# Kernel tuning notes

Hardware: AMD Instinct MI355X
Metric: run time of the kernel (lower is better)

Reference implementation:

```python
import jax, jax.numpy as jnp
import numpy as np

MARGIN = 0.2
NEG_INF = -1e30
POS_INF = 1e30


def setup_inputs() -> dict:
    key = jax.random.key(0)
    k1, k2 = jax.random.split(key)
    B, D = 8192, 128
    im = jax.random.normal(k1, (B, D), dtype=jnp.float32)
    ids = jax.random.randint(k2, (B,), 0, 512, dtype=jnp.int64)
    return {"im": im, "ids": ids}


def reference(im, ids):
    # scores[i, j] = <im_i, im_j>, with the diagonal zeroed (as in the original,
    # which sets scores[j][j] = 0 before mining). Note the positive set includes
    # the anchor itself, so min over positives includes the zeroed diagonal.
    B = im.shape[0]
    scores = im @ im.T                      # [B, B]
    scores = scores * (1.0 - jnp.eye(B, dtype=scores.dtype))
    pos_mask = ids[:, None] == ids[None, :]  # same id (includes self)
    neg_mask = ~pos_mask
    max_neg = jnp.max(jnp.where(neg_mask, scores, NEG_INF), axis=1)  # hardest negative per anchor
    min_pos = jnp.min(jnp.where(pos_mask, scores, POS_INF), axis=1)  # hardest positive per anchor
    cost = jnp.sum(jnp.maximum(MARGIN + max_neg - min_pos, 0.0))
    return cost
```

## Files before the change

kernel.cpp:

```cpp
#include <hip/hip_runtime.h>
#include <hip/hip_bf16.h>

#define MARGIN  0.2f
#define NEG_INF -1e30f
#define POS_INF 1e30f

#define B_SZ 8192
#define D_SZ 128
#define CS   16
#define BLK_COLS 512
#define PHASE_COLS 64
#define NPH (BLK_COLS / PHASE_COLS)

typedef __bf16 bf16x8 __attribute__((ext_vector_type(8)));
typedef __bf16 bf16x4 __attribute__((ext_vector_type(4)));
typedef float  f32x4  __attribute__((ext_vector_type(4)));

__global__ __launch_bounds__(256) void k_convert(const float* __restrict__ in,
                                                 __bf16* __restrict__ out) {
    int i = (blockIdx.x * 256 + threadIdx.x) * 4;
    float4 v = *reinterpret_cast<const float4*>(in + i);
    bf16x4 o;
    o[0] = (__bf16)v.x; o[1] = (__bf16)v.y; o[2] = (__bf16)v.z; o[3] = (__bf16)v.w;
    *reinterpret_cast<bf16x4*>(out + i) = o;
}

__global__ __launch_bounds__(256, 3) void k_mine(const __bf16* __restrict__ imb,
                                                 const int* __restrict__ ids,
                                                 float* __restrict__ wsmax,
                                                 float* __restrict__ wsmin) {
    __shared__ __bf16 bpanel[2][PHASE_COLS * D_SZ];
    __shared__ int    ids_s[BLK_COLS];

    const int bid = blockIdx.x;
    const int wg  = (bid & 7) * 64 + (bid >> 3);
    const int rb  = wg & 31;
    const int cs  = wg >> 5;

    const int tid  = threadIdx.x;
    const int w    = tid >> 6;
    const int lane = tid & 63;
    const int quad = lane >> 4;
    const int lr   = lane & 15;

    const int rowbase = rb * 256 + w * 64;
    const int col0    = cs * BLK_COLS;

    bf16x8 afrag[4][4];
    #pragma unroll
    for (int s = 0; s < 4; ++s) {
        const __bf16* p = imb + (size_t)(rowbase + s * 16 + lr) * D_SZ + quad * 8;
        #pragma unroll
        for (int kf = 0; kf < 4; ++kf)
            afrag[s][kf] = *reinterpret_cast<const bf16x8*>(p + kf * 32);
    }

    int rid[4][4];
    #pragma unroll
    for (int s = 0; s < 4; ++s)
        #pragma unroll
        for (int r = 0; r < 4; ++r)
            rid[s][r] = ids[rowbase + s * 16 + quad * 4 + r];

    int2 myids = *reinterpret_cast<const int2*>(ids + col0 + tid * 2);
    *reinterpret_cast<int2*>(&ids_s[tid * 2]) = myids;

    {
        const __bf16* src = imb + (size_t)(col0 + w * 16 + lr) * D_SZ + quad * 8;
        #pragma unroll
        for (int kf = 0; kf < 4; ++kf)
            __builtin_amdgcn_global_load_lds(
                (const __attribute__((address_space(1))) unsigned int*)(src + kf * 32),
                (__attribute__((address_space(3))) unsigned int*)(&bpanel[0][(w * 4 + kf) * 512]),
                16, 0, 0);
    }
    asm volatile("s_waitcnt vmcnt(0) lgkmcnt(0)" ::: "memory");
    __builtin_amdgcn_s_barrier();

    float mxn[4][4], mnp[4][4];
    #pragma unroll
    for (int s = 0; s < 4; ++s)
        #pragma unroll
        for (int r = 0; r < 4; ++r) { mxn[s][r] = NEG_INF; mnp[s][r] = POS_INF; }

    #pragma unroll 1
    for (int p = 0; p < NPH; ++p) {
        if (p + 1 < NPH) {
            const int nbuf = (p + 1) & 1;
            const __bf16* src = imb + (size_t)(col0 + (p + 1) * PHASE_COLS + w * 16 + lr) * D_SZ + quad * 8;
            #pragma unroll
            for (int kf = 0; kf < 4; ++kf)
                __builtin_amdgcn_global_load_lds(
                    (const __attribute__((address_space(1))) unsigned int*)(src + kf * 32),
                    (__attribute__((address_space(3))) unsigned int*)(&bpanel[nbuf][(w * 4 + kf) * 512]),
                    16, 0, 0);
        }
        const int buf = p & 1;
        #pragma unroll 1
        for (int tt = 0; tt < 4; ++tt) {
            const int cid = ids_s[p * PHASE_COLS + tt * 16 + lr];
            bf16x8 bfr[4];
            const __bf16* bp = &bpanel[buf][tt * 4 * 512] + lane * 8;
            #pragma unroll
            for (int kf = 0; kf < 4; ++kf)
                bfr[kf] = *reinterpret_cast<const bf16x8*>(bp + kf * 512);
            #pragma unroll
            for (int s = 0; s < 4; ++s) {
                f32x4 acc = {0.f, 0.f, 0.f, 0.f};
                #pragma unroll
                for (int kf = 0; kf < 4; ++kf)
                    acc = __builtin_amdgcn_mfma_f32_16x16x32_bf16(afrag[s][kf], bfr[kf], acc, 0, 0, 0);
                #pragma unroll
                for (int r = 0; r < 4; ++r) {
                    float sv   = acc[r];
                    bool  same = (rid[s][r] == cid);
                    mxn[s][r] = fmaxf(mxn[s][r], same ? NEG_INF : sv);
                    mnp[s][r] = fminf(mnp[s][r], same ? sv : POS_INF);
                }
            }
        }
        asm volatile("s_waitcnt vmcnt(0) lgkmcnt(0)" ::: "memory");
        __builtin_amdgcn_s_barrier();
    }

    #pragma unroll
    for (int s = 0; s < 4; ++s)
        #pragma unroll
        for (int r = 0; r < 4; ++r) {
            float mx = mxn[s][r];
            float mn = mnp[s][r];
            #pragma unroll
            for (int m = 1; m < 16; m <<= 1) {
                mx = fmaxf(mx, __shfl_xor(mx, m, 64));
                mn = fminf(mn, __shfl_xor(mn, m, 64));
            }
            if (lr == 0) {
                int row = rowbase + s * 16 + quad * 4 + r;
                wsmax[(size_t)row * CS + cs] = mx;
                wsmin[(size_t)row * CS + cs] = mn;
            }
        }
}

__global__ __launch_bounds__(256) void k_final(const float* __restrict__ wsmax,
                                               const float* __restrict__ wsmin,
                                               float* __restrict__ out) {
    int r = blockIdx.x * 256 + threadIdx.x;
    float mx = NEG_INF;
    float mn = 0.0f;
    #pragma unroll
    for (int c = 0; c < CS; c += 4) {
        f32x4 vx = *reinterpret_cast<const f32x4*>(wsmax + (size_t)r * CS + c);
        f32x4 vn = *reinterpret_cast<const f32x4*>(wsmin + (size_t)r * CS + c);
        mx = fmaxf(mx, fmaxf(fmaxf(vx[0], vx[1]), fmaxf(vx[2], vx[3])));
        mn = fminf(mn, fminf(fminf(vn[0], vn[1]), fminf(vn[2], vn[3])));
    }
    float cost = fmaxf(MARGIN + mx - mn, 0.0f);
    #pragma unroll
    for (int m = 1; m < 64; m <<= 1)
        cost += __shfl_xor(cost, m, 64);
    __shared__ float part[4];
    if ((threadIdx.x & 63) == 0) part[threadIdx.x >> 6] = cost;
    __syncthreads();
    if (threadIdx.x == 0)
        atomicAdd(out, part[0] + part[1] + part[2] + part[3]);
}

extern "C" void kernel_launch(void* const* d_in, const int* in_sizes, int n_in,
                              void* d_out, int out_size, void* d_ws, size_t ws_size,
                              hipStream_t stream) {
    const float* im  = (const float*)d_in[0];
    const int*   ids = (const int*)d_in[1];
    float*       out = (float*)d_out;

    __bf16* imb   = (__bf16*)d_ws;
    float*  wsmax = (float*)((char*)d_ws + (size_t)B_SZ * D_SZ * 2);
    float*  wsmin = wsmax + (size_t)B_SZ * CS;

    hipMemsetAsync(d_out, 0, sizeof(float), stream);

    k_convert<<<(B_SZ * D_SZ) / (256 * 4), 256, 0, stream>>>(im, imb);
    k_mine<<<32 * CS, 256, 0, stream>>>(imb, ids, wsmax, wsmin);
    k_final<<<B_SZ / 256, 256, 0, stream>>>(wsmax, wsmin, out);
}
```

Before: 100.4 us.

## Switch mining kernel to 32x32x16 MFMA with 128-row blocks

Replaces the 16x16x32 MFMA tiling with 32x32x16 bf16 MFMA. Each wave now owns 32 rows with 16 accumulator values, and blocks cover 128 rows, so the grid doubles to 1024 workgroups. The B-panel LDS layout and ids mapping are reworked to match the 32x32 fragment layout, and the tt loop is unrolled. The aim is fewer MFMA issues per output plus more blocks for occupancy, at the cost of reloading the B panel for twice as many row blocks. The convert kernel also widens to 8 elements per thread and the final kernel uses 128-thread blocks.

Result: no change. 98.60 us (-1.8%).

```diff
diff --git a/kernel.cpp b/kernel.cpp
--- a/kernel.cpp
+++ b/kernel.cpp
@@ -13,16 +13,18 @@
 #define NPH (BLK_COLS / PHASE_COLS)
 
 typedef __bf16 bf16x8 __attribute__((ext_vector_type(8)));
-typedef __bf16 bf16x4 __attribute__((ext_vector_type(4)));
 typedef float  f32x4  __attribute__((ext_vector_type(4)));
+typedef float  f32x16 __attribute__((ext_vector_type(16)));
 
 __global__ __launch_bounds__(256) void k_convert(const float* __restrict__ in,
                                                  __bf16* __restrict__ out) {
-    int i = (blockIdx.x * 256 + threadIdx.x) * 4;
-    float4 v = *reinterpret_cast<const float4*>(in + i);
-    bf16x4 o;
-    o[0] = (__bf16)v.x; o[1] = (__bf16)v.y; o[2] = (__bf16)v.z; o[3] = (__bf16)v.w;
-    *reinterpret_cast<bf16x4*>(out + i) = o;
+    int i = (blockIdx.x * 256 + threadIdx.x) * 8;
+    float4 v0 = *reinterpret_cast<const float4*>(in + i);
+    float4 v1 = *reinterpret_cast<const float4*>(in + i + 4);
+    bf16x8 o;
+    o[0] = (__bf16)v0.x; o[1] = (__bf16)v0.y; o[2] = (__bf16)v0.z; o[3] = (__bf16)v0.w;
+    o[4] = (__bf16)v1.x; o[5] = (__bf16)v1.y; o[6] = (__bf16)v1.z; o[7] = (__bf16)v1.w;
+    *reinterpret_cast<bf16x8*>(out + i) = o;
 }
 
 __global__ __launch_bounds__(256, 3) void k_mine(const __bf16* __restrict__ imb,
@@ -33,90 +35,85 @@
     __shared__ int    ids_s[BLK_COLS];
 
     const int bid = blockIdx.x;
-    const int wg  = (bid & 7) * 64 + (bid >> 3);
-    const int rb  = wg & 31;
-    const int cs  = wg >> 5;
+    const int wg  = (bid & 7) * 128 + (bid >> 3);
+    const int rb  = wg & 63;
+    const int cs  = wg >> 6;
 
     const int tid  = threadIdx.x;
     const int w    = tid >> 6;
     const int lane = tid & 63;
-    const int quad = lane >> 4;
-    const int lr   = lane & 15;
+    const int half = lane >> 5;
+    const int l5   = lane & 31;
 
-    const int rowbase = rb * 256 + w * 64;
+    const int rowbase = rb * 128 + w * 32;
     const int col0    = cs * BLK_COLS;
 
-    bf16x8 afrag[4][4];
-    #pragma unroll
-    for (int s = 0; s < 4; ++s) {
-        const __bf16* p = imb + (size_t)(rowbase + s * 16 + lr) * D_SZ + quad * 8;
+    const int s_tile = w >> 1;
+    const int s_kf0  = (w & 1) * 4;
+
+    {
+        const __bf16* src = imb + (size_t)(col0 + s_tile * 32 + l5) * D_SZ + s_kf0 * 16 + half * 8;
         #pragma unroll
-        for (int kf = 0; kf < 4; ++kf)
-            afrag[s][kf] = *reinterpret_cast<const bf16x8*>(p + kf * 32);
+        for (int j = 0; j < 4; ++j)
+            __builtin_amdgcn_global_load_lds(
+                (const __attribute__((address_space(1))) unsigned int*)(src + j * 16),
+                (__attribute__((address_space(3))) unsigned int*)(&bpanel[0][(s_tile * 8 + s_kf0 + j) * 512]),
+                16, 0, 0);
     }
 
-    int rid[4][4];
+    bf16x8 afrag[8];
+    {
+        const __bf16* p = imb + (size_t)(rowbase + l5) * D_SZ + half * 8;
+        #pragma unroll
+        for (int kf = 0; kf < 8; ++kf)
+            afrag[kf] = *reinterpret_cast<const bf16x8*>(p + kf * 16);
+    }
+
+    int rid[16];
     #pragma unroll
-    for (int s = 0; s < 4; ++s)
-        #pragma unroll
-        for (int r = 0; r < 4; ++r)
-            rid[s][r] = ids[rowbase + s * 16 + quad * 4 + r];
+    for (int r = 0; r < 16; ++r)
+        rid[r] = ids[rowbase + (r & 3) + 8 * (r >> 2) + 4 * half];
 
-    int2 myids = *reinterpret_cast<const int2*>(ids + col0 + tid * 2);
-    *reinterpret_cast<int2*>(&ids_s[tid * 2]) = myids;
+    *reinterpret_cast<int2*>(&ids_s[tid * 2]) =
+        *reinterpret_cast<const int2*>(ids + col0 + tid * 2);
 
-    {
-        const __bf16* src = imb + (size_t)(col0 + w * 16 + lr) * D_SZ + quad * 8;
-        #pragma unroll
-        for (int kf = 0; kf < 4; ++kf)
-            __builtin_amdgcn_global_load_lds(
-                (const __attribute__((address_space(1))) unsigned int*)(src + kf * 32),
-                (__attribute__((address_space(3))) unsigned int*)(&bpanel[0][(w * 4 + kf) * 512]),
-                16, 0, 0);
-    }
     asm volatile("s_waitcnt vmcnt(0) lgkmcnt(0)" ::: "memory");
     __builtin_amdgcn_s_barrier();
 
-    float mxn[4][4], mnp[4][4];
+    float mxn[16], mnp[16];
     #pragma unroll
-    for (int s = 0; s < 4; ++s)
-        #pragma unroll
-        for (int r = 0; r < 4; ++r) { mxn[s][r] = NEG_INF; mnp[s][r] = POS_INF; }
+    for (int r = 0; r < 16; ++r) { mxn[r] = NEG_INF; mnp[r] = POS_INF; }
 
     #pragma unroll 1
     for (int p = 0; p < NPH; ++p) {
         if (p + 1 < NPH) {
             const int nbuf = (p + 1) & 1;
-            const __bf16* src = imb + (size_t)(col0 + (p + 1) * PHASE_COLS + w * 16 + lr) * D_SZ + quad * 8;
+            const __bf16* src = imb + (size_t)(col0 + (p + 1) * PHASE_COLS + s_tile * 32 + l5) * D_SZ
+                                + s_kf0 * 16 + half * 8;
             #pragma unroll
-            for (int kf = 0; kf < 4; ++kf)
+            for (int j = 0; j < 4; ++j)
                 __builtin_amdgcn_global_load_lds(
-                    (const __attribute__((address_space(1))) unsigned int*)(src + kf * 32),
-                    (__attribute__((address_space(3))) unsigned int*)(&bpanel[nbuf][(w * 4 + kf) * 512]),
+                    (const __attribute__((address_space(1))) unsigned int*)(src + j * 16),
+                    (__attribute__((address_space(3))) unsigned int*)(&bpanel[nbuf][(s_tile * 8 + s_kf0 + j) * 512]),
                     16, 0, 0);
         }
         const int buf = p & 1;
-        #pragma unroll 1
-        for (int tt = 0; tt < 4; ++tt) {
-            const int cid = ids_s[p * PHASE_COLS + tt * 16 + lr];
-            bf16x8 bfr[4];
-            const __bf16* bp = &bpanel[buf][tt * 4 * 512] + lane * 8;
+        #pragma unroll
+        for (int t = 0; t < 2; ++t) {
+            const __bf16* bbase = &bpanel[buf][t * 4096] + (size_t)lane * 8;
+            f32x16 acc = {};
             #pragma unroll
-            for (int kf = 0; kf < 4; ++kf)
-                bfr[kf] = *reinterpret_cast<const bf16x8*>(bp + kf * 512);
+            for (int kf = 0; kf < 8; ++kf) {
+                bf16x8 bfr = *reinterpret_cast<const bf16x8*>(bbase + kf * 512);
+                acc = __builtin_amdgcn_mfma_f32_32x32x16_bf16(afrag[kf], bfr, acc, 0, 0, 0);
+            }
+            const int cid = ids_s[p * PHASE_COLS + t * 32 + l5];
             #pragma unroll
-            for (int s = 0; s < 4; ++s) {
-                f32x4 acc = {0.f, 0.f, 0.f, 0.f};
-                #pragma unroll
-                for (int kf = 0; kf < 4; ++kf)
-                    acc = __builtin_amdgcn_mfma_f32_16x16x32_bf16(afrag[s][kf], bfr[kf], acc, 0, 0, 0);
-                #pragma unroll
-                for (int r = 0; r < 4; ++r) {
-                    float sv   = acc[r];
-                    bool  same = (rid[s][r] == cid);
-                    mxn[s][r] = fmaxf(mxn[s][r], same ? NEG_INF : sv);
-                    mnp[s][r] = fminf(mnp[s][r], same ? sv : POS_INF);
-                }
+            for (int r = 0; r < 16; ++r) {
+                float sv   = acc[r];
+                bool  same = (rid[r] == cid);
+                mxn[r] = fmaxf(mxn[r], same ? NEG_INF : sv);
+                mnp[r] = fminf(mnp[r], same ? sv : POS_INF);
             }
         }
         asm volatile("s_waitcnt vmcnt(0) lgkmcnt(0)" ::: "memory");
@@ -124,28 +121,26 @@
     }
 
     #pragma unroll
-    for (int s = 0; s < 4; ++s)
+    for (int r = 0; r < 16; ++r) {
+        float mx = mxn[r];
+        float mn = mnp[r];
         #pragma unroll
-        for (int r = 0; r < 4; ++r) {
-            float mx = mxn[s][r];
-            float mn = mnp[s][r];
-            #pragma unroll
-            for (int m = 1; m < 16; m <<= 1) {
-                mx = fmaxf(mx, __shfl_xor(mx, m, 64));
-                mn = fminf(mn, __shfl_xor(mn, m, 64));
-            }
-            if (lr == 0) {
-                int row = rowbase + s * 16 + quad * 4 + r;
-                wsmax[(size_t)row * CS + cs] = mx;
-                wsmin[(size_t)row * CS + cs] = mn;
-            }
+        for (int m = 1; m < 32; m <<= 1) {
+            mx = fmaxf(mx, __shfl_xor(mx, m, 64));
+            mn = fminf(mn, __shfl_xor(mn, m, 64));
         }
+        if (l5 == 0) {
+            int row = rowbase + (r & 3) + 8 * (r >> 2) + 4 * half;
+            wsmax[(size_t)row * CS + cs] = mx;
+            wsmin[(size_t)row * CS + cs] = mn;
+        }
+    }
 }
 
-__global__ __launch_bounds__(256) void k_final(const float* __restrict__ wsmax,
+__global__ __launch_bounds__(128) void k_final(const float* __restrict__ wsmax,
                                                const float* __restrict__ wsmin,
                                                float* __restrict__ out) {
-    int r = blockIdx.x * 256 + threadIdx.x;
+    int r = blockIdx.x * 128 + threadIdx.x;
     float mx = NEG_INF;
     float mn = 0.0f;
     #pragma unroll
@@ -159,11 +154,11 @@
     #pragma unroll
     for (int m = 1; m < 64; m <<= 1)
         cost += __shfl_xor(cost, m, 64);
-    __shared__ float part[4];
+    __shared__ float part[2];
     if ((threadIdx.x & 63) == 0) part[threadIdx.x >> 6] = cost;
     __syncthreads();
     if (threadIdx.x == 0)
-        atomicAdd(out, part[0] + part[1] + part[2] + part[3]);
+        atomicAdd(out, part[0] + part[1]);
 }
 
 extern "C" void kernel_launch(void* const* d_in, const int* in_sizes, int n_in,
@@ -179,7 +174,7 @@
 
     hipMemsetAsync(d_out, 0, sizeof(float), stream);
 
-    k_convert<<<(B_SZ * D_SZ) / (256 * 4), 256, 0, stream>>>(im, imb);
-    k_mine<<<32 * CS, 256, 0, stream>>>(imb, ids, wsmax, wsmin);
-    k_final<<<B_SZ / 256, 256, 0, stream>>>(wsmax, wsmin, out);
+    k_convert<<<(B_SZ * D_SZ) / (256 * 8), 256, 0, stream>>>(im, imb);
+    k_mine<<<64 * CS, 256, 0, stream>>>(imb, ids, wsmax, wsmin);
+    k_final<<<B_SZ / 128, 128, 0, stream>>>(wsmax, wsmin, out);
 }
```
